# Optimization experiments

Hardware: AMD Instinct MI355X
Metric: run time of the kernel (lower is better)

Reference implementation:

```python
import jax, jax.numpy as jnp
import numpy as np

N = 50000   # nodes
E = 600000  # directed edges
B = 128     # graphs
IN = 128
H = 128
K = 30      # sort-pool k
C_OUT = 32
KER = 5
OUT_DIM = 10
L_OUT = K - KER + 1  # 26


def setup_inputs() -> dict:
    key = jax.random.key(0)
    ks = jax.random.split(key, 12)
    s = 0.05
    return {
        "x": jax.random.normal(ks[0], (N, IN), jnp.float32),
        "edge_index": jax.random.randint(ks[1], (2, E), 0, N),
        "batch": jnp.sort(jax.random.randint(ks[2], (N,), 0, B)),
        "W0": jax.random.normal(ks[3], (IN, H), jnp.float32) * s,
        "b0": jnp.zeros((H,), jnp.float32),
        "W1": jax.random.normal(ks[4], (H, H), jnp.float32) * s,
        "b1": jnp.zeros((H,), jnp.float32),
        "W2": jax.random.normal(ks[5], (H, H), jnp.float32) * s,
        "b2": jnp.zeros((H,), jnp.float32),
        "conv_w": jax.random.normal(ks[6], (C_OUT, H, KER), jnp.float32) * s,
        "conv_b": jnp.zeros((C_OUT,), jnp.float32),
        "lin1_w": jax.random.normal(ks[7], (C_OUT * L_OUT, H), jnp.float32) * s,
        "lin1_b": jnp.zeros((H,), jnp.float32),
        "lin2_w": jax.random.normal(ks[8], (H, OUT_DIM), jnp.float32) * s,
        "lin2_b": jnp.zeros((OUT_DIM,), jnp.float32),
    }


def reference(x, edge_index, batch, W0, b0, W1, b1, W2, b2,
              conv_w, conv_b, lin1_w, lin1_b, lin2_w, lin2_b):
    # --- GCN normalization (A + I, symmetric deg^-1/2) ---
    loops = jnp.arange(N)
    row = jnp.concatenate([edge_index[0], loops])  # source
    col = jnp.concatenate([edge_index[1], loops])  # target (aggregation side)
    deg = jax.ops.segment_sum(jnp.ones_like(col, dtype=x.dtype), col, num_segments=N)
    dinv = jax.lax.rsqrt(jnp.maximum(deg, 1.0))
    norm = dinv[row] * dinv[col]  # [E+N]

    def gcn(h, W, b):
        hw = h @ W                                            # [N,H]
        msg = hw[row] * norm[:, None]                         # gather [E+N,H]
        return jax.ops.segment_sum(msg, col, num_segments=N) + b

    h = jax.nn.relu(gcn(x, W0, b0))
    h = jax.nn.relu(gcn(h, W1, b1))
    h = jax.nn.relu(gcn(h, W2, b2))

    # --- SortAggregation: per-graph sort by last channel (desc), top-K, zero-pad ---
    last = h[:, -1]
    order = jnp.lexsort((-last, batch))  # primary: batch, secondary: last desc
    hs = h[order]
    bs = batch[order]
    counts = jax.ops.segment_sum(jnp.ones((N,), jnp.int32), batch, num_segments=B)
    starts = jnp.cumsum(counts) - counts  # exclusive prefix sum
    rank = jnp.arange(N) - starts[bs]     # within-graph rank after sort
    r = jnp.where(rank < K, rank, K)      # overflow bucket K is discarded
    pooled = jnp.zeros((B, K + 1, H), h.dtype).at[bs, r].add(hs)[:, :K]  # [B,K,H]

    # --- conv1d head (NCH layout, matches torch view/transpose) ---
    xc = jnp.transpose(pooled, (0, 2, 1))  # [B,H,K]
    y = jax.lax.conv_general_dilated(xc, conv_w, (1,), "VALID",
                                     dimension_numbers=("NCH", "OIH", "NCH"))
    y = jax.nn.relu(y + conv_b[None, :, None])  # [B,C_OUT,L_OUT]
    y = y.reshape(B, -1)
    y = jax.nn.relu(y @ lin1_w + lin1_b)
    return y @ lin2_w + lin2_b  # [B,OUT_DIM]
```

## Files before the change

### kernel.cpp

```cpp
#include <hip/hip_runtime.h>
#include <math.h>

#define Nn 50000
#define Ee 600000
#define Bg 128
#define Hd 128
#define Kt 30
#define CO 32
#define KW 5
#define LOUT 26
#define CAP 2048
#define SCB 196
#define MMB 782

typedef float v2f __attribute__((ext_vector_type(2)));
typedef short bf16x8 __attribute__((ext_vector_type(8)));
typedef float f32x4 __attribute__((ext_vector_type(4)));

__device__ __forceinline__ unsigned short bfr(float v) {
    unsigned u = __builtin_bit_cast(unsigned, v);
    unsigned r = (u + 0x7FFFu + ((u >> 16) & 1u)) >> 16;
    return (unsigned short)r;
}
__device__ __forceinline__ float bff(unsigned short h) {
    unsigned u = ((unsigned)h) << 16;
    return __builtin_bit_cast(float, u);
}

__global__ void countpack_kernel(const int* __restrict__ ei, const int* __restrict__ batch,
                            int* __restrict__ deg_i, int* __restrict__ bstart,
                            const float* __restrict__ conv_w, float* __restrict__ wT2,
                            const float* __restrict__ W0, const float* __restrict__ W1,
                            const float* __restrict__ W2,
                            ushort* __restrict__ Bph, ushort* __restrict__ Bpm,
                            ushort* __restrict__ Bpl) {
    int i = blockIdx.x * 256 + threadIdx.x;
    if (i < Ee) atomicAdd(&deg_i[ei[Ee + i]], 1);
    if (i < Nn) {
        int b = batch[i];
        if (i == 0) bstart[b] = 0;
        else if (batch[i - 1] != b) bstart[b] = i;
    }
    if (i == 0) bstart[Bg] = Nn;
    if (i < CO * KW * Hd) {
        int ci = i & 127;
        int r = i >> 7;
        int o = r / KW, k = r - o * KW;
        wT2[i] = conv_w[((size_t)o * Hd + ci) * KW + k];
    }
    if (i < 3 * 2048) {
        int l = i >> 11;
        int r = i & 2047;
        int kc = r >> 9;
        int n = (r >> 6) & 7;
        int lane = r & 63;
        int m = lane & 15, kq = lane >> 4;
        const float* W = (l == 0) ? W0 : (l == 1) ? W1 : W2;
        int col = n * 16 + m;
        size_t off = ((size_t)l * 2048 + (size_t)((kc * 8 + n) * 64 + lane)) * 8;
#pragma unroll
        for (int j = 0; j < 8; ++j) {
            float v = W[(size_t)(kc * 32 + kq * 8 + j) * Hd + col];
            unsigned short h = bfr(v);
            float r1 = v - bff(h);
            unsigned short mid = bfr(r1);
            Bph[off + j] = h;
            Bpm[off + j] = mid;
            Bpl[off + j] = bfr(r1 - bff(mid));
        }
    }
}

__global__ __launch_bounds__(256) void scanBC2_kernel(const int* __restrict__ deg_i,
                            int* __restrict__ row_ptr, float* __restrict__ dinv,
                            int* __restrict__ bstart) {
    __shared__ int ls[256];
    __shared__ int boffS;
    int tid = threadIdx.x;
    int b = blockIdx.x;
    int s = 0;
    for (int k = 0; k < b; ++k)
        s += deg_i[k * 256 + tid] + 1;
    ls[tid] = s;
    __syncthreads();
    for (int off = 128; off > 0; off >>= 1) {
        if (tid < off) ls[tid] += ls[tid + off];
        __syncthreads();
    }
    if (tid == 0) boffS = ls[0];
    __syncthreads();
    int boff = boffS;
    int i = b * 256 + tid;
    int v2 = 0;
    if (i < Nn) {
        int raw = deg_i[i];
        v2 = raw + 1;
        dinv[i] = 1.0f / sqrtf((float)(raw + 2));
    }
    ls[tid] = v2;
    __syncthreads();
    for (int off = 1; off < 256; off <<= 1) {
        int t = (tid >= off) ? ls[tid - off] : 0;
        __syncthreads();
        ls[tid] += t;
        __syncthreads();
    }
    if (i < Nn) row_ptr[i + 1] = ls[tid] + boff;
    if (i == 0) row_ptr[0] = 0;
    if (b == 0 && tid == 0) {
        for (int bb = Bg - 1; bb >= 0; --bb)
            if (bstart[bb] == -1) bstart[bb] = bstart[bb + 1];
    }
}

__device__ __forceinline__ void mmx_body(int bid, int tid,
                            const float* __restrict__ Hin,
                            const ushort* __restrict__ Bph, const ushort* __restrict__ Bpm,
                            const ushort* __restrict__ Bpl,
                            const float* __restrict__ dinv, float* __restrict__ hw) {
    int w = tid >> 6, lane = tid & 63;
    int m = lane & 15, kq = lane >> 4;
    int rowA = bid * 64 + w * 16 + m;
    bool va = rowA < Nn;
    const float* ap = Hin + (size_t)rowA * Hd;
    f32x4 acc[8];
#pragma unroll
    for (int n = 0; n < 8; ++n) acc[n] = (f32x4)0.f;
#pragma unroll
    for (int kc = 0; kc < 4; ++kc) {
        bf16x8 a0 = (bf16x8)0, a1 = (bf16x8)0, a2 = (bf16x8)0;
        if (va) {
            float av[8];
            *(float4*)&av[0] = *(const float4*)(ap + kc * 32 + kq * 8);
            *(float4*)&av[4] = *(const float4*)(ap + kc * 32 + kq * 8 + 4);
#pragma unroll
            for (int j = 0; j < 8; ++j) {
                unsigned short h = bfr(av[j]);
                float r1 = av[j] - bff(h);
                unsigned short mid = bfr(r1);
                a0[j] = (short)h;
                a1[j] = (short)mid;
                a2[j] = (short)bfr(r1 - bff(mid));
            }
        }
        const ushort* bhp = Bph + (size_t)((kc * 8) * 64 + lane) * 8;
        const ushort* bmp = Bpm + (size_t)((kc * 8) * 64 + lane) * 8;
        const ushort* blp = Bpl + (size_t)((kc * 8) * 64 + lane) * 8;
#pragma unroll
        for (int n = 0; n < 8; ++n) {
            bf16x8 b0 = *(const bf16x8*)(bhp + (size_t)n * 64 * 8);
            bf16x8 b1 = *(const bf16x8*)(bmp + (size_t)n * 64 * 8);
            bf16x8 b2 = *(const bf16x8*)(blp + (size_t)n * 64 * 8);
            acc[n] = __builtin_amdgcn_mfma_f32_16x16x32_bf16(a0, b0, acc[n], 0, 0, 0);
            acc[n] = __builtin_amdgcn_mfma_f32_16x16x32_bf16(a1, b0, acc[n], 0, 0, 0);
            acc[n] = __builtin_amdgcn_mfma_f32_16x16x32_bf16(a0, b1, acc[n], 0, 0, 0);
            acc[n] = __builtin_amdgcn_mfma_f32_16x16x32_bf16(a1, b1, acc[n], 0, 0, 0);
            acc[n] = __builtin_amdgcn_mfma_f32_16x16x32_bf16(a2, b0, acc[n], 0, 0, 0);
            acc[n] = __builtin_amdgcn_mfma_f32_16x16x32_bf16(a0, b2, acc[n], 0, 0, 0);
        }
    }
    int rbase = bid * 64 + w * 16 + kq * 4;
#pragma unroll
    for (int reg = 0; reg < 4; ++reg) {
        int r = rbase + reg;
        if (r < Nn) {
            float s = dinv[r];
#pragma unroll
            for (int n = 0; n < 8; ++n)
                hw[(size_t)r * Hd + n * 16 + m] = acc[n][reg] * s;
        }
    }
}

__global__ __launch_bounds__(256) void mmx_kernel(const float* __restrict__ Hin,
                            const ushort* __restrict__ Bph, const ushort* __restrict__ Bpm,
                            const ushort* __restrict__ Bpl,
                            const float* __restrict__ dinv, float* __restrict__ hw) {
    mmx_body(blockIdx.x, threadIdx.x, Hin, Bph, Bpm, Bpl, dinv, hw);
}

__global__ __launch_bounds__(256) void mmxfill_kernel(const float* __restrict__ Hin,
                            const ushort* __restrict__ Bph, const ushort* __restrict__ Bpm,
                            const ushort* __restrict__ Bpl,
                            const float* __restrict__ dinv, float* __restrict__ hw,
                            const int* __restrict__ ei, const int* __restrict__ row_ptr,
                            int* __restrict__ cnt, int* __restrict__ csr_src) {
    if (blockIdx.x < MMB) {
        mmx_body(blockIdx.x, threadIdx.x, Hin, Bph, Bpm, Bpl, dinv, hw);
    } else {
        int e = (blockIdx.x - MMB) * 256 + threadIdx.x;
        if (e < Ee) {
            int c = ei[Ee + e];
            int r = ei[e];
            int p = row_ptr[c] + atomicAdd(&cnt[c], 1) + 1;
            csr_src[p] = r;
        }
    }
}

__global__ __launch_bounds__(256) void agg_kernel(const float* __restrict__ hw,
                            const int* __restrict__ row_ptr, const int* __restrict__ csr_src,
                            const float* __restrict__ dinv, const float* __restrict__ bias,
                            float* __restrict__ hout) {
    int node = blockIdx.x * 4 + (threadIdx.x >> 6);
    if (node >= Nn) return;
    int lane = threadIdx.x & 63;
    const v2f* hw2 = (const v2f*)hw;
    v2f a0 = hw2[(size_t)node * 64 + lane];
    v2f a1 = 0.f, a2 = 0.f, a3 = 0.f;
    int e0 = row_ptr[node], e1 = row_ptr[node + 1];
    int e = e0;
    for (; e + 3 < e1; e += 4) {
        int s0 = __builtin_nontemporal_load(csr_src + e);
        int s1 = __builtin_nontemporal_load(csr_src + e + 1);
        int s2 = __builtin_nontemporal_load(csr_src + e + 2);
        int s3 = __builtin_nontemporal_load(csr_src + e + 3);
        a0 += hw2[(size_t)s0 * 64 + lane];
        a1 += hw2[(size_t)s1 * 64 + lane];
        a2 += hw2[(size_t)s2 * 64 + lane];
        a3 += hw2[(size_t)s3 * 64 + lane];
    }
    for (; e < e1; ++e) {
        int s0 = __builtin_nontemporal_load(csr_src + e);
        a0 += hw2[(size_t)s0 * 64 + lane];
    }
    v2f acc = (a0 + a1) + (a2 + a3);
    float d = dinv[node];
    v2f bv = ((const v2f*)bias)[lane];
    v2f o;
    o.x = fmaxf(fmaf(d, acc.x, bv.x), 0.f);
    o.y = fmaxf(fmaf(d, acc.y, bv.y), 0.f);
    ((v2f*)hout)[(size_t)node * 64 + lane] = o;
}

__global__ __launch_bounds__(1024) void tail_kernel(const float* __restrict__ h,
                            const int* __restrict__ bstart,
                            const float* __restrict__ wT2, const float* __restrict__ conv_b,
                            const float* __restrict__ l1w, const float* __restrict__ l1b,
                            const float* __restrict__ l2w, const float* __restrict__ l2b,
                            float* __restrict__ out) {
    __shared__ float vals[CAP];
    __shared__ float xcl[Kt][130];
    __shared__ float fl[CO * LOUT];
    __shared__ float pz[8][Hd];
    __shared__ float z[Hd];
    __shared__ int selS[Kt];
    int b = blockIdx.x, tid = threadIdx.x;

    int s0 = bstart[b], s1 = bstart[b + 1];
    int n = s1 - s0;
    int nc = n < CAP ? n : CAP;
    if (tid < Kt) selS[tid] = -1;
    for (int j = tid; j < nc; j += 1024)
        vals[j] = h[(size_t)(s0 + j) * Hd + (Hd - 1)];
    __syncthreads();

    for (int j = tid; j < nc; j += 1024) {
        float vj = vals[j];
        int rank = 0;
        for (int i = 0; i < nc; ++i) {
            float vi = vals[i];
            rank += (vi > vj || (vi == vj && i < j)) ? 1 : 0;
        }
        if (rank < Kt) selS[rank] = s0 + j;
    }
    __syncthreads();

    for (int i = tid; i < Kt * Hd; i += 1024) {
        int t = i >> 7, c = i & 127;
        int s = selS[t];
        xcl[t][c] = (s >= 0) ? h[(size_t)s * Hd + c] : 0.f;
    }
    __syncthreads();
    if (tid < CO * LOUT) {
        int o = tid / LOUT, t = tid - o * LOUT;
        float acc = conv_b[o];
#pragma unroll
        for (int k = 0; k < KW; ++k) {
            const float* xr = &xcl[t + k][0];
            const float* wr = wT2 + ((size_t)o * KW + k) * Hd;
#pragma unroll 8
            for (int c4 = 0; c4 < 32; ++c4) {
                float2 xa = *(const float2*)(xr + c4 * 4);
                float2 xb = *(const float2*)(xr + c4 * 4 + 2);
                float4 wv = *(const float4*)(wr + c4 * 4);
                acc = fmaf(xa.x, wv.x, acc);
                acc = fmaf(xa.y, wv.y, acc);
                acc = fmaf(xb.x, wv.z, acc);
                acc = fmaf(xb.y, wv.w, acc);
            }
        }
        fl[tid] = fmaxf(acc, 0.f);
    }
    __syncthreads();
    int hh = tid & 127, chunk = tid >> 7;
    int m0 = chunk * 104;
    float acc = 0.f;
    const float* lw = l1w + (size_t)m0 * Hd + hh;
#pragma unroll 8
    for (int m = 0; m < 104; ++m)
        acc = fmaf(fl[m0 + m], lw[(size_t)m * Hd], acc);
    pz[chunk][hh] = acc;
    __syncthreads();
    if (tid < Hd) {
        float a = l1b[tid];
#pragma unroll
        for (int q = 0; q < 8; ++q) a += pz[q][tid];
        z[tid] = fmaxf(a, 0.f);
    }
    __syncthreads();
    if (tid < 10) {
        float a2 = l2b[tid];
        for (int j = 0; j < Hd; ++j)
            a2 = fmaf(z[j], l2w[j * 10 + tid], a2);
        out[b * 10 + tid] = a2;
    }
}

extern "C" void kernel_launch(void* const* d_in, const int* in_sizes, int n_in,
                              void* d_out, int out_size, void* d_ws, size_t ws_size,
                              hipStream_t stream) {
    const float* x      = (const float*)d_in[0];
    const int*   ei     = (const int*)d_in[1];
    const int*   batch  = (const int*)d_in[2];
    const float* W0     = (const float*)d_in[3];
    const float* b0     = (const float*)d_in[4];
    const float* W1     = (const float*)d_in[5];
    const float* b1     = (const float*)d_in[6];
    const float* W2     = (const float*)d_in[7];
    const float* b2     = (const float*)d_in[8];
    const float* conv_w = (const float*)d_in[9];
    const float* conv_b = (const float*)d_in[10];
    const float* l1w    = (const float*)d_in[11];
    const float* l1b    = (const float*)d_in[12];
    const float* l2w    = (const float*)d_in[13];
    const float* l2b    = (const float*)d_in[14];
    float* out = (float*)d_out;

    int* wsI = (int*)d_ws;
    size_t off = 0;
    int*   deg_i   = wsI + off; off += Nn;
    int*   cnt     = wsI + off; off += Nn;
    int*   bstart  = wsI + off; off += 132;
    int*   row_ptr = wsI + off; off += 50004;
    float* dinv    = (float*)(wsI + off); off += Nn;
    int*   csr_src = wsI + off; off += Ee;
    off = (off + 3) & ~(size_t)3;
    ushort* Bph  = (ushort*)(wsI + off); off += 3 * 16384 / 2;
    ushort* Bpm  = (ushort*)(wsI + off); off += 3 * 16384 / 2;
    ushort* Bpl  = (ushort*)(wsI + off); off += 3 * 16384 / 2;
    float* hw    = (float*)(wsI + off); off += (size_t)Nn * Hd;
    float* hbuf  = (float*)(wsI + off); off += (size_t)Nn * Hd;
    float* wT2   = (float*)(wsI + off); off += CO * KW * Hd;

    hipMemsetAsync(deg_i, 0xFF, (size_t)(Nn + Nn + 132) * 4, stream);
    countpack_kernel<<<(Ee + 255) / 256, 256, 0, stream>>>(ei, batch, deg_i, bstart,
        conv_w, wT2, W0, W1, W2, Bph, Bpm, Bpl);
    scanBC2_kernel<<<SCB, 256, 0, stream>>>(deg_i, row_ptr, dinv, bstart);
    dim3 aggGrid((Nn + 3) / 4);
    mmxfill_kernel<<<MMB + (Ee + 255) / 256, 256, 0, stream>>>(x, Bph, Bpm, Bpl,
        dinv, hw, ei, row_ptr, cnt, csr_src);
    agg_kernel<<<aggGrid, 256, 0, stream>>>(hw, row_ptr, csr_src, dinv, b0, hbuf);
    mmx_kernel<<<MMB, 256, 0, stream>>>(hbuf, Bph + 16384, Bpm + 16384, Bpl + 16384, dinv, hw);
    agg_kernel<<<aggGrid, 256, 0, stream>>>(hw, row_ptr, csr_src, dinv, b1, hbuf);
    mmx_kernel<<<MMB, 256, 0, stream>>>(hbuf, Bph + 32768, Bpm + 32768, Bpl + 32768, dinv, hw);
    agg_kernel<<<aggGrid, 256, 0, stream>>>(hw, row_ptr, csr_src, dinv, b2, hbuf);
    tail_kernel<<<Bg, 1024, 0, stream>>>(hbuf, bstart, wT2, conv_b,
                                         l1w, l1b, l2w, l2b, out);
}
```

Before: 444.6 us.

## Fuse GCN aggregation with next layer's bf16x3 MFMA matmul via LDS tile

Adds an aggmm kernel in which each block aggregates neighbor features for 64 nodes, applying bias and ReLU, and writes them into an LDS tile. It then runs the next layer's split-bf16 MFMA matmul directly from that tile and writes the dinv-scaled output. This removes the full N×H intermediate write and read, plus one launch per layer, for layers 1 and 2. In exchange, the gather phase gets far fewer blocks (782 instead of 12500), each wave processes 16 nodes serially, and LDS use per block limits occupancy, which could reduce latency hiding in the gather.

```diff
diff --git a/kernel.cpp b/kernel.cpp
--- a/kernel.cpp
+++ b/kernel.cpp
@@ -170,13 +170,6 @@
                 hw[(size_t)r * Hd + n * 16 + m] = acc[n][reg] * s;
         }
     }
-}
-
-__global__ __launch_bounds__(256) void mmx_kernel(const float* __restrict__ Hin,
-                            const ushort* __restrict__ Bph, const ushort* __restrict__ Bpm,
-                            const ushort* __restrict__ Bpl,
-                            const float* __restrict__ dinv, float* __restrict__ hw) {
-    mmx_body(blockIdx.x, threadIdx.x, Hin, Bph, Bpm, Bpl, dinv, hw);
 }
 
 __global__ __launch_bounds__(256) void mmxfill_kernel(const float* __restrict__ Hin,
@@ -194,6 +187,97 @@
             int r = ei[e];
             int p = row_ptr[c] + atomicAdd(&cnt[c], 1) + 1;
             csr_src[p] = r;
+        }
+    }
+}
+
+__global__ __launch_bounds__(256) void aggmm_kernel(const float* __restrict__ hwin,
+                            const int* __restrict__ row_ptr, const int* __restrict__ csr_src,
+                            const float* __restrict__ dinv, const float* __restrict__ bias,
+                            const ushort* __restrict__ Bph, const ushort* __restrict__ Bpm,
+                            const ushort* __restrict__ Bpl,
+                            float* __restrict__ hwout) {
+    __shared__ __align__(16) float At[64][132];
+    int tid = threadIdx.x;
+    int w = tid >> 6, lane = tid & 63;
+    int bid = blockIdx.x;
+    const v2f* hw2 = (const v2f*)hwin;
+    v2f bv = ((const v2f*)bias)[lane];
+    for (int t = 0; t < 16; ++t) {
+        int rl = w * 16 + t;
+        int node = bid * 64 + rl;
+        v2f o = (v2f)0.f;
+        if (node < Nn) {
+            v2f a0 = hw2[(size_t)node * 64 + lane];
+            v2f a1 = (v2f)0.f, a2 = (v2f)0.f, a3 = (v2f)0.f;
+            int e0 = row_ptr[node], e1 = row_ptr[node + 1];
+            int e = e0;
+            for (; e + 3 < e1; e += 4) {
+                int s0 = __builtin_nontemporal_load(csr_src + e);
+                int s1 = __builtin_nontemporal_load(csr_src + e + 1);
+                int s2 = __builtin_nontemporal_load(csr_src + e + 2);
+                int s3 = __builtin_nontemporal_load(csr_src + e + 3);
+                a0 += hw2[(size_t)s0 * 64 + lane];
+                a1 += hw2[(size_t)s1 * 64 + lane];
+                a2 += hw2[(size_t)s2 * 64 + lane];
+                a3 += hw2[(size_t)s3 * 64 + lane];
+            }
+            for (; e < e1; ++e) {
+                int s0 = __builtin_nontemporal_load(csr_src + e);
+                a0 += hw2[(size_t)s0 * 64 + lane];
+            }
+            v2f acc = (a0 + a1) + (a2 + a3);
+            float d = dinv[node];
+            o.x = fmaxf(fmaf(d, acc.x, bv.x), 0.f);
+            o.y = fmaxf(fmaf(d, acc.y, bv.y), 0.f);
+        }
+        *(v2f*)&At[rl][lane * 2] = o;
+    }
+    int m = lane & 15, kq = lane >> 4;
+    f32x4 acc[8];
+#pragma unroll
+    for (int n = 0; n < 8; ++n) acc[n] = (f32x4)0.f;
+    const float* arow = &At[w * 16 + m][0];
+#pragma unroll
+    for (int kc = 0; kc < 4; ++kc) {
+        bf16x8 a0, a1, a2;
+        float av[8];
+        *(float4*)&av[0] = *(const float4*)(arow + kc * 32 + kq * 8);
+        *(float4*)&av[4] = *(const float4*)(arow + kc * 32 + kq * 8 + 4);
+#pragma unroll
+        for (int j = 0; j < 8; ++j) {
+            unsigned short h = bfr(av[j]);
+            float r1 = av[j] - bff(h);
+            unsigned short mid = bfr(r1);
+            a0[j] = (short)h;
+            a1[j] = (short)mid;
+            a2[j] = (short)bfr(r1 - bff(mid));
+        }
+        const ushort* bhp = Bph + (size_t)((kc * 8) * 64 + lane) * 8;
+        const ushort* bmp = Bpm + (size_t)((kc * 8) * 64 + lane) * 8;
+        const ushort* blp = Bpl + (size_t)((kc * 8) * 64 + lane) * 8;
+#pragma unroll
+        for (int n = 0; n < 8; ++n) {
+            bf16x8 b0 = *(const bf16x8*)(bhp + (size_t)n * 64 * 8);
+            bf16x8 b1 = *(const bf16x8*)(bmp + (size_t)n * 64 * 8);
+            bf16x8 b2 = *(const bf16x8*)(blp + (size_t)n * 64 * 8);
+            acc[n] = __builtin_amdgcn_mfma_f32_16x16x32_bf16(a0, b0, acc[n], 0, 0, 0);
+            acc[n] = __builtin_amdgcn_mfma_f32_16x16x32_bf16(a1, b0, acc[n], 0, 0, 0);
+            acc[n] = __builtin_amdgcn_mfma_f32_16x16x32_bf16(a0, b1, acc[n], 0, 0, 0);
+            acc[n] = __builtin_amdgcn_mfma_f32_16x16x32_bf16(a1, b1, acc[n], 0, 0, 0);
+            acc[n] = __builtin_amdgcn_mfma_f32_16x16x32_bf16(a2, b0, acc[n], 0, 0, 0);
+            acc[n] = __builtin_amdgcn_mfma_f32_16x16x32_bf16(a0, b2, acc[n], 0, 0, 0);
+        }
+    }
+    int rbase = bid * 64 + w * 16 + kq * 4;
+#pragma unroll
+    for (int reg = 0; reg < 4; ++reg) {
+        int r = rbase + reg;
+        if (r < Nn) {
+            float s = dinv[r];
+#pragma unroll
+            for (int n = 0; n < 8; ++n)
+                hwout[(size_t)r * Hd + n * 16 + m] = acc[n][reg] * s;
         }
     }
 }
@@ -360,10 +444,10 @@
     dim3 aggGrid((Nn + 3) / 4);
     mmxfill_kernel<<<MMB + (Ee + 255) / 256, 256, 0, stream>>>(x, Bph, Bpm, Bpl,
         dinv, hw, ei, row_ptr, cnt, csr_src);
-    agg_kernel<<<aggGrid, 256, 0, stream>>>(hw, row_ptr, csr_src, dinv, b0, hbuf);
-    mmx_kernel<<<MMB, 256, 0, stream>>>(hbuf, Bph + 16384, Bpm + 16384, Bpl + 16384, dinv, hw);
-    agg_kernel<<<aggGrid, 256, 0, stream>>>(hw, row_ptr, csr_src, dinv, b1, hbuf);
-    mmx_kernel<<<MMB, 256, 0, stream>>>(hbuf, Bph + 32768, Bpm + 32768, Bpl + 32768, dinv, hw);
+    aggmm_kernel<<<MMB, 256, 0, stream>>>(hw, row_ptr, csr_src, dinv, b0,
+        Bph + 16384, Bpm + 16384, Bpl + 16384, hbuf);
+    aggmm_kernel<<<MMB, 256, 0, stream>>>(hbuf, row_ptr, csr_src, dinv, b1,
+        Bph + 32768, Bpm + 32768, Bpl + 32768, hw);
     agg_kernel<<<aggGrid, 256, 0, stream>>>(hw, row_ptr, csr_src, dinv, b2, hbuf);
     tail_kernel<<<Bg, 1024, 0, stream>>>(hbuf, bstart, wT2, conv_b,
                                          l1w, l1b, l2w, l2b, out);
```

Measured after the change: 466.7 us. 5.0% more time.
